# Kernel optimization log

Hardware: AMD Instinct MI355X
Metric: run time of the kernel (lower is better)

The kernel has to match this reference:

```python
import jax, jax.numpy as jnp
import numpy as np

N_NODES = 50000
E_G = 1600000   # edges of g = nodes of line graph h
E_H = 2000000   # edges of line graph h (triplets)
IN_FEATS = 64
N_COLORS = 4


def setup_inputs() -> dict:
    key = jax.random.key(0)
    k1, k2, k3, k4, k5, k6, k7, k8 = jax.random.split(key, 8)
    return {
        "h_nodes": jax.random.randint(k1, (N_NODES,), 0, N_COLORS, dtype=jnp.int32),
        "src_g": jax.random.randint(k2, (E_G,), 0, N_NODES, dtype=jnp.int32),
        "dst_g": jax.random.randint(k3, (E_G,), 0, N_NODES, dtype=jnp.int32),
        "src_h": jax.random.randint(k4, (E_H,), 0, E_G, dtype=jnp.int32),
        "dst_h": jax.random.randint(k5, (E_H,), 0, E_G, dtype=jnp.int32),
        "e1_w": jax.random.normal(k6, (2, IN_FEATS), dtype=jnp.float32),
        "e2_w": jax.random.normal(k7, (2, IN_FEATS), dtype=jnp.float32),
        "e3_w": jax.random.normal(k8, (2, IN_FEATS), dtype=jnp.float32),
    }


def reference(h_nodes, src_g, dst_g, src_h, dst_h, e1_w, e2_w, e3_w):
    # g.apply_edges(send_h_src): per g-edge gather of node colors
    h_src = h_nodes[src_g]   # [E_G] color at source node of each g-edge
    h_dst = h_nodes[dst_g]   # [E_G] color at dest node of each g-edge
    # line graph h: its nodes are g's edges; apply_edges(comparison3)
    ha = h_src[src_h]        # [E_H] src-edge's source color (a)
    hc = h_dst[dst_h]        # [E_H] dst-edge's dest color (c)
    hb = h_dst[src_h]        # [E_H] src-edge's dest color (b = shared node)
    hac = (ha == hc).astype(jnp.int32)
    hab = (ha == hb).astype(jnp.int32)
    hbc = (hc == hb).astype(jnp.int32)
    # three size-2 embedding lookups + sum -> [E_H, IN_FEATS]
    return e1_w[hac] + e2_w[hab] + e3_w[hbc]
```

## Files before the change

kernel.cpp:

```cpp
#include <hip/hip_runtime.h>
#include <hip/hip_bf16.h>

__global__ void __launch_bounds__(256)
pack_edge_colors_kernel(const int4* __restrict__ src_g4,
                        const int4* __restrict__ dst_g4,
                        const int* __restrict__ src_g,
                        const int* __restrict__ dst_g,
                        const int* __restrict__ h_nodes,
                        unsigned char* __restrict__ pc,
                        int eg) {
    const int n4 = eg >> 2;
    const int stride = gridDim.x * blockDim.x;
    for (int i = blockIdx.x * blockDim.x + threadIdx.x; i < n4; i += stride) {
        int4 s = src_g4[i];
        int4 d = dst_g4[i];
        uchar4 p;
        p.x = (unsigned char)((h_nodes[s.x] << 2) | h_nodes[d.x]);
        p.y = (unsigned char)((h_nodes[s.y] << 2) | h_nodes[d.y]);
        p.z = (unsigned char)((h_nodes[s.z] << 2) | h_nodes[d.z]);
        p.w = (unsigned char)((h_nodes[s.w] << 2) | h_nodes[d.w]);
        *(uchar4*)(pc + (i << 2)) = p;
    }
    int t = blockIdx.x * blockDim.x + threadIdx.x;
    int e = (n4 << 2) + t;
    if (e < eg) {
        pc[e] = (unsigned char)((h_nodes[src_g[e]] << 2) | h_nodes[dst_g[e]]);
    }
}

#define ROWS_PER_TILE 256

__global__ void __launch_bounds__(256)
triplet_out_kernel(const int* __restrict__ src_h,
                   const int* __restrict__ dst_h,
                   const unsigned char* __restrict__ pc,
                   const float* __restrict__ e1,
                   const float* __restrict__ e2,
                   const float* __restrict__ e3,
                   float4* __restrict__ out4,
                   int eh) {
    __shared__ float table[8 * 64];
    __shared__ unsigned char combo_s[ROWS_PER_TILE];

    const int tid = threadIdx.x;

    for (int i = tid; i < 8 * 64; i += blockDim.x) {
        int combo = i >> 6;
        int f     = i & 63;
        table[i] = e1[((combo >> 2) & 1) * 64 + f]
                 + e2[((combo >> 1) & 1) * 64 + f]
                 + e3[( combo       & 1) * 64 + f];
    }
    __syncthreads();

    const float4* table4 = (const float4*)table;

    for (long long base = (long long)blockIdx.x * ROWS_PER_TILE; base < eh;
         base += (long long)gridDim.x * ROWS_PER_TILE) {
        long long row = base + tid;
        if (row < eh) {
            int s = src_h[row];
            int d = dst_h[row];
            unsigned int ps = pc[s];
            unsigned int pd = pc[d];
            int a = (int)(ps >> 2);
            int b = (int)(ps & 3u);
            int c = (int)(pd & 3u);
            combo_s[tid] =
                (unsigned char)(((a == c) << 2) | ((a == b) << 1) | (int)(b == c));
        }
        __syncthreads();

        int nrows = eh - base < ROWS_PER_TILE ? (int)(eh - base) : ROWS_PER_TILE;
        int total4 = nrows << 4;
        for (int j = tid; j < total4; j += blockDim.x) {
            int rl   = j >> 4;
            int lane = j & 15;
            out4[(base + rl) * 16 + lane] = table4[combo_s[rl] * 16 + lane];
        }
        __syncthreads();
    }
}

extern "C" void kernel_launch(void* const* d_in, const int* in_sizes, int n_in,
                              void* d_out, int out_size, void* d_ws, size_t ws_size,
                              hipStream_t stream) {
    const int* h_nodes = (const int*)d_in[0];
    const int* src_g   = (const int*)d_in[1];
    const int* dst_g   = (const int*)d_in[2];
    const int* src_h   = (const int*)d_in[3];
    const int* dst_h   = (const int*)d_in[4];
    const float* e1_w  = (const float*)d_in[5];
    const float* e2_w  = (const float*)d_in[6];
    const float* e3_w  = (const float*)d_in[7];

    const int eg = in_sizes[1];
    const int eh = in_sizes[3];

    unsigned char* pc = (unsigned char*)d_ws;

    pack_edge_colors_kernel<<<2048, 256, 0, stream>>>(
        (const int4*)src_g, (const int4*)dst_g, src_g, dst_g, h_nodes, pc, eg);

    triplet_out_kernel<<<2048, 256, 0, stream>>>(src_h, dst_h, pc,
                                                 e1_w, e2_w, e3_w,
                                                 (float4*)d_out, eh);
}
```

Measured before the change: 561.2 us.

## Prefetch next tile's combos during output writes and use nontemporal stores

Software-pipelines the triplet kernel so each thread computes the next tile's combo code (index loads plus gather from the packed color array) while the current tile's output rows are being written. Output and packed-color writes become nontemporal stores, so the large streaming output avoids polluting the cache. The pack kernel's grid is halved. The combo gather latency is meant to overlap the write-bound phase. The price is a slightly more complex loop, plus the risk that nontemporal stores behave differently on this memory system.

```diff
diff --git a/kernel.cpp b/kernel.cpp
--- a/kernel.cpp
+++ b/kernel.cpp
@@ -1,5 +1,7 @@
 #include <hip/hip_runtime.h>
 #include <hip/hip_bf16.h>
+
+typedef float nfloat4 __attribute__((ext_vector_type(4)));
 
 __global__ void __launch_bounds__(256)
 pack_edge_colors_kernel(const int4* __restrict__ src_g4,
@@ -14,12 +16,12 @@
     for (int i = blockIdx.x * blockDim.x + threadIdx.x; i < n4; i += stride) {
         int4 s = src_g4[i];
         int4 d = dst_g4[i];
-        uchar4 p;
-        p.x = (unsigned char)((h_nodes[s.x] << 2) | h_nodes[d.x]);
-        p.y = (unsigned char)((h_nodes[s.y] << 2) | h_nodes[d.y]);
-        p.z = (unsigned char)((h_nodes[s.z] << 2) | h_nodes[d.z]);
-        p.w = (unsigned char)((h_nodes[s.w] << 2) | h_nodes[d.w]);
-        *(uchar4*)(pc + (i << 2)) = p;
+        unsigned int p =
+            (unsigned int)((h_nodes[s.x] << 2) | h_nodes[d.x])
+          | ((unsigned int)((h_nodes[s.y] << 2) | h_nodes[d.y]) << 8)
+          | ((unsigned int)((h_nodes[s.z] << 2) | h_nodes[d.z]) << 16)
+          | ((unsigned int)((h_nodes[s.w] << 2) | h_nodes[d.w]) << 24);
+        __builtin_nontemporal_store(p, (unsigned int*)(pc + (i << 2)));
     }
     int t = blockIdx.x * blockDim.x + threadIdx.x;
     int e = (n4 << 2) + t;
@@ -28,7 +30,7 @@
     }
 }
 
-#define ROWS_PER_TILE 256
+#define TILE 256
 
 __global__ void __launch_bounds__(256)
 triplet_out_kernel(const int* __restrict__ src_h,
@@ -37,10 +39,10 @@
                    const float* __restrict__ e1,
                    const float* __restrict__ e2,
                    const float* __restrict__ e3,
-                   float4* __restrict__ out4,
+                   float* __restrict__ out,
                    int eh) {
     __shared__ float table[8 * 64];
-    __shared__ unsigned char combo_s[ROWS_PER_TILE];
+    __shared__ unsigned char combo_s[TILE];
 
     const int tid = threadIdx.x;
 
@@ -51,13 +53,15 @@
                  + e2[((combo >> 1) & 1) * 64 + f]
                  + e3[( combo       & 1) * 64 + f];
     }
-    __syncthreads();
 
-    const float4* table4 = (const float4*)table;
+    const nfloat4* table4 = (const nfloat4*)table;
+    nfloat4* out4 = (nfloat4*)out;
+    const long long ntiles = ((long long)eh + TILE - 1) / TILE;
 
-    for (long long base = (long long)blockIdx.x * ROWS_PER_TILE; base < eh;
-         base += (long long)gridDim.x * ROWS_PER_TILE) {
-        long long row = base + tid;
+    long long t = blockIdx.x;
+    unsigned char my_combo = 0;
+    if (t < ntiles) {
+        long long row = t * TILE + tid;
         if (row < eh) {
             int s = src_h[row];
             int d = dst_h[row];
@@ -66,18 +70,41 @@
             int a = (int)(ps >> 2);
             int b = (int)(ps & 3u);
             int c = (int)(pd & 3u);
-            combo_s[tid] =
-                (unsigned char)(((a == c) << 2) | ((a == b) << 1) | (int)(b == c));
+            my_combo = (unsigned char)(((a == c) << 2) | ((a == b) << 1) |
+                                       (int)(b == c));
         }
+    }
+    __syncthreads();
+
+    while (t < ntiles) {
+        combo_s[tid] = my_combo;
         __syncthreads();
 
-        int nrows = eh - base < ROWS_PER_TILE ? (int)(eh - base) : ROWS_PER_TILE;
+        long long t_next = t + gridDim.x;
+        if (t_next < ntiles) {
+            long long row = t_next * TILE + tid;
+            if (row < eh) {
+                int s = src_h[row];
+                int d = dst_h[row];
+                unsigned int ps = pc[s];
+                unsigned int pd = pc[d];
+                int a = (int)(ps >> 2);
+                int b = (int)(ps & 3u);
+                int c = (int)(pd & 3u);
+                my_combo = (unsigned char)(((a == c) << 2) | ((a == b) << 1) |
+                                           (int)(b == c));
+            }
+        }
+
+        long long base = t * TILE;
+        int nrows = (eh - base) < TILE ? (int)(eh - base) : TILE;
         int total4 = nrows << 4;
         for (int j = tid; j < total4; j += blockDim.x) {
-            int rl   = j >> 4;
-            int lane = j & 15;
-            out4[(base + rl) * 16 + lane] = table4[combo_s[rl] * 16 + lane];
+            nfloat4 v = table4[combo_s[j >> 4] * 16 + (j & 15)];
+            __builtin_nontemporal_store(v, &out4[base * 16 + j]);
         }
+
+        t = t_next;
         __syncthreads();
     }
 }
@@ -99,10 +126,10 @@
 
     unsigned char* pc = (unsigned char*)d_ws;
 
-    pack_edge_colors_kernel<<<2048, 256, 0, stream>>>(
+    pack_edge_colors_kernel<<<1024, 256, 0, stream>>>(
         (const int4*)src_g, (const int4*)dst_g, src_g, dst_g, h_nodes, pc, eg);
 
     triplet_out_kernel<<<2048, 256, 0, stream>>>(src_h, dst_h, pc,
                                                  e1_w, e2_w, e3_w,
-                                                 (float4*)d_out, eh);
+                                                 (float*)d_out, eh);
 }
```

New measurement: 558.7 us, median of 2. No clear change (-0.4%).

## Split triplet kernel into combo pass and register-table streaming output pass

Applied to the files above, without the earlier changes.

The fused triplet kernel is split into two. The first pass computes a one-byte combo code per triplet using vectorized int4 index loads. The second pass streams the output with nontemporal stores, building each row from embedding rows held in registers, so it no longer needs a shared-memory table or block barriers. The cost is an extra kernel launch and a 2 MB intermediate combo round trip in exchange for a pure streaming write loop; the pack kernel also switches to nontemporal packed stores with fewer blocks.

```diff
diff --git a/kernel.cpp b/kernel.cpp
--- a/kernel.cpp
+++ b/kernel.cpp
@@ -1,5 +1,7 @@
 #include <hip/hip_runtime.h>
 #include <hip/hip_bf16.h>
+
+typedef float nfloat4 __attribute__((ext_vector_type(4)));
 
 __global__ void __launch_bounds__(256)
 pack_edge_colors_kernel(const int4* __restrict__ src_g4,
@@ -14,12 +16,12 @@
     for (int i = blockIdx.x * blockDim.x + threadIdx.x; i < n4; i += stride) {
         int4 s = src_g4[i];
         int4 d = dst_g4[i];
-        uchar4 p;
-        p.x = (unsigned char)((h_nodes[s.x] << 2) | h_nodes[d.x]);
-        p.y = (unsigned char)((h_nodes[s.y] << 2) | h_nodes[d.y]);
-        p.z = (unsigned char)((h_nodes[s.z] << 2) | h_nodes[d.z]);
-        p.w = (unsigned char)((h_nodes[s.w] << 2) | h_nodes[d.w]);
-        *(uchar4*)(pc + (i << 2)) = p;
+        unsigned int p =
+            (unsigned int)((h_nodes[s.x] << 2) | h_nodes[d.x])
+          | ((unsigned int)((h_nodes[s.y] << 2) | h_nodes[d.y]) << 8)
+          | ((unsigned int)((h_nodes[s.z] << 2) | h_nodes[d.z]) << 16)
+          | ((unsigned int)((h_nodes[s.w] << 2) | h_nodes[d.w]) << 24);
+        __builtin_nontemporal_store(p, (unsigned int*)(pc + (i << 2)));
     }
     int t = blockIdx.x * blockDim.x + threadIdx.x;
     int e = (n4 << 2) + t;
@@ -28,57 +30,75 @@
     }
 }
 
-#define ROWS_PER_TILE 256
+__global__ void __launch_bounds__(256)
+combo_kernel(const int4* __restrict__ src_h4,
+             const int4* __restrict__ dst_h4,
+             const int* __restrict__ src_h,
+             const int* __restrict__ dst_h,
+             const unsigned char* __restrict__ pc,
+             unsigned char* __restrict__ combo,
+             int eh) {
+    const int n4 = eh >> 2;
+    const int stride = gridDim.x * blockDim.x;
+    const int tid = blockIdx.x * blockDim.x + threadIdx.x;
+
+    for (int i = tid; i < n4; i += stride) {
+        int4 s = src_h4[i];
+        int4 d = dst_h4[i];
+        unsigned int ps0 = pc[s.x], pd0 = pc[d.x];
+        unsigned int ps1 = pc[s.y], pd1 = pc[d.y];
+        unsigned int ps2 = pc[s.z], pd2 = pc[d.z];
+        unsigned int ps3 = pc[s.w], pd3 = pc[d.w];
+        unsigned int cw = 0;
+        {
+            int a = ps0 >> 2, b = ps0 & 3, c = pd0 & 3;
+            cw |= (unsigned int)(((a == c) << 2) | ((a == b) << 1) | (b == c));
+        }
+        {
+            int a = ps1 >> 2, b = ps1 & 3, c = pd1 & 3;
+            cw |= (unsigned int)(((a == c) << 2) | ((a == b) << 1) | (b == c)) << 8;
+        }
+        {
+            int a = ps2 >> 2, b = ps2 & 3, c = pd2 & 3;
+            cw |= (unsigned int)(((a == c) << 2) | ((a == b) << 1) | (b == c)) << 16;
+        }
+        {
+            int a = ps3 >> 2, b = ps3 & 3, c = pd3 & 3;
+            cw |= (unsigned int)(((a == c) << 2) | ((a == b) << 1) | (b == c)) << 24;
+        }
+        __builtin_nontemporal_store(cw, (unsigned int*)(combo + (i << 2)));
+    }
+    int e = (n4 << 2) + tid;
+    if (e < eh) {
+        unsigned int ps = pc[src_h[e]], pd = pc[dst_h[e]];
+        int a = ps >> 2, b = ps & 3, c = pd & 3;
+        combo[e] = (unsigned char)(((a == c) << 2) | ((a == b) << 1) | (b == c));
+    }
+}
 
 __global__ void __launch_bounds__(256)
-triplet_out_kernel(const int* __restrict__ src_h,
-                   const int* __restrict__ dst_h,
-                   const unsigned char* __restrict__ pc,
-                   const float* __restrict__ e1,
-                   const float* __restrict__ e2,
-                   const float* __restrict__ e3,
-                   float4* __restrict__ out4,
-                   int eh) {
-    __shared__ float table[8 * 64];
-    __shared__ unsigned char combo_s[ROWS_PER_TILE];
+stream_out_kernel(const unsigned char* __restrict__ combo,
+                  const float* __restrict__ e1,
+                  const float* __restrict__ e2,
+                  const float* __restrict__ e3,
+                  nfloat4* __restrict__ out4,
+                  long long total4) {
+    const int lane = threadIdx.x & 15;
+    const nfloat4 e1a = ((const nfloat4*)e1)[lane];
+    const nfloat4 e1b = ((const nfloat4*)e1)[16 + lane];
+    const nfloat4 e2a = ((const nfloat4*)e2)[lane];
+    const nfloat4 e2b = ((const nfloat4*)e2)[16 + lane];
+    const nfloat4 e3a = ((const nfloat4*)e3)[lane];
+    const nfloat4 e3b = ((const nfloat4*)e3)[16 + lane];
 
-    const int tid = threadIdx.x;
-
-    for (int i = tid; i < 8 * 64; i += blockDim.x) {
-        int combo = i >> 6;
-        int f     = i & 63;
-        table[i] = e1[((combo >> 2) & 1) * 64 + f]
-                 + e2[((combo >> 1) & 1) * 64 + f]
-                 + e3[( combo       & 1) * 64 + f];
-    }
-    __syncthreads();
-
-    const float4* table4 = (const float4*)table;
-
-    for (long long base = (long long)blockIdx.x * ROWS_PER_TILE; base < eh;
-         base += (long long)gridDim.x * ROWS_PER_TILE) {
-        long long row = base + tid;
-        if (row < eh) {
-            int s = src_h[row];
-            int d = dst_h[row];
-            unsigned int ps = pc[s];
-            unsigned int pd = pc[d];
-            int a = (int)(ps >> 2);
-            int b = (int)(ps & 3u);
-            int c = (int)(pd & 3u);
-            combo_s[tid] =
-                (unsigned char)(((a == c) << 2) | ((a == b) << 1) | (int)(b == c));
-        }
-        __syncthreads();
-
-        int nrows = eh - base < ROWS_PER_TILE ? (int)(eh - base) : ROWS_PER_TILE;
-        int total4 = nrows << 4;
-        for (int j = tid; j < total4; j += blockDim.x) {
-            int rl   = j >> 4;
-            int lane = j & 15;
-            out4[(base + rl) * 16 + lane] = table4[combo_s[rl] * 16 + lane];
-        }
-        __syncthreads();
+    const long long stride = (long long)gridDim.x * blockDim.x;
+    for (long long j = (long long)blockIdx.x * blockDim.x + threadIdx.x;
+         j < total4; j += stride) {
+        unsigned int c = combo[j >> 4];
+        nfloat4 v = (c & 4u ? e1b : e1a)
+                  + (c & 2u ? e2b : e2a)
+                  + (c & 1u ? e3b : e3a);
+        __builtin_nontemporal_store(v, &out4[j]);
     }
 }
 
@@ -97,12 +117,16 @@
     const int eg = in_sizes[1];
     const int eh = in_sizes[3];
 
-    unsigned char* pc = (unsigned char*)d_ws;
+    unsigned char* pc    = (unsigned char*)d_ws;
+    unsigned char* combo = (unsigned char*)d_ws + (1 << 21);
 
-    pack_edge_colors_kernel<<<2048, 256, 0, stream>>>(
+    pack_edge_colors_kernel<<<1024, 256, 0, stream>>>(
         (const int4*)src_g, (const int4*)dst_g, src_g, dst_g, h_nodes, pc, eg);
 
-    triplet_out_kernel<<<2048, 256, 0, stream>>>(src_h, dst_h, pc,
-                                                 e1_w, e2_w, e3_w,
-                                                 (float4*)d_out, eh);
+    combo_kernel<<<2048, 256, 0, stream>>>(
+        (const int4*)src_h, (const int4*)dst_h, src_h, dst_h, pc, combo, eh);
+
+    const long long total4 = (long long)eh * 16;
+    stream_out_kernel<<<2048, 256, 0, stream>>>(
+        combo, e1_w, e2_w, e3_w, (nfloat4*)d_out, total4);
 }
```

Result: slower. 577.3 us (+2.9%).
